# Performance work log

Hardware: AMD Instinct MI355X
Metric: run time of the kernel (lower is better)

Reference implementation:

```python
import jax, jax.numpy as jnp
import numpy as np

B, S, D, H, F = 2, 2048, 1024, 16, 4096
HD = D // H
EPS = 1e-5


def _layernorm(x, g, b):
    mu = jnp.mean(x, axis=-1, keepdims=True)
    var = jnp.var(x, axis=-1, keepdims=True)
    return (x - mu) * jax.lax.rsqrt(var + EPS) * g + b


def setup_inputs() -> dict:
    key = jax.random.key(0)
    ks = jax.random.split(key, 10)
    sd = 0.02
    return {
        "src": jax.random.normal(ks[0], (B, S, D), jnp.float32),
        "qkv_w": jax.random.normal(ks[1], (3 * D, D), jnp.float32) * sd,
        "qkv_b": jnp.zeros((3 * D,), jnp.float32),
        "out_w": jax.random.normal(ks[2], (D, D), jnp.float32) * sd,
        "out_b": jnp.zeros((D,), jnp.float32),
        "ffn_w1": jax.random.normal(ks[3], (F, D), jnp.float32) * sd,
        "ffn_b1": jnp.zeros((F,), jnp.float32),
        "ffn_w2": jax.random.normal(ks[4], (D, F), jnp.float32) * sd,
        "ffn_b2": jnp.zeros((D,), jnp.float32),
        "ln1_g": jnp.ones((D,), jnp.float32),
        "ln1_b": jnp.zeros((D,), jnp.float32),
        "ln2_g": jnp.ones((D,), jnp.float32),
        "ln2_b": jnp.zeros((D,), jnp.float32),
    }


def reference(src, qkv_w, qkv_b, out_w, out_b, ffn_w1, ffn_b1, ffn_w2, ffn_b2,
              ln1_g, ln1_b, ln2_g, ln2_b):
    # --- Multi-head self-attention (post-norm, dropout=identity in eval) ---
    qkv = src @ qkv_w.T + qkv_b                        # [B,S,3D]
    qkv = qkv.reshape(B, S, H, 3 * HD).transpose(0, 2, 1, 3)  # [B,H,S,3hd]
    q, k, v = jnp.split(qkv, 3, axis=-1)               # each [B,H,S,hd]
    scores = jnp.einsum('bhqd,bhkd->bhqk', q, k) / np.sqrt(HD).astype(np.float32)
    attn = jax.nn.softmax(scores, axis=-1)
    ctx = jnp.einsum('bhqk,bhkd->bhqd', attn, v)       # [B,H,S,hd]
    ctx = ctx.transpose(0, 2, 1, 3).reshape(B, S, D)
    mha_out = ctx @ out_w.T + out_b
    agg = _layernorm(src + mha_out, ln1_g, ln1_b)
    # --- FFN: Linear -> ReLU -> Linear ---
    h = jax.nn.relu(agg @ ffn_w1.T + ffn_b1)
    ffn_out = h @ ffn_w2.T + ffn_b2
    return _layernorm(agg + ffn_out, ln2_g, ln2_b)
```

## Files before the change

### kernel.cpp

```cpp
#include <hip/hip_runtime.h>


typedef unsigned short u16;
typedef unsigned int u32;
typedef __attribute__((ext_vector_type(8))) __bf16 bf16x8;
typedef __attribute__((ext_vector_type(4))) float f32x4;
typedef __attribute__((ext_vector_type(4))) short s16x4;
typedef __attribute__((ext_vector_type(2))) u32 u32x2;

__device__ __forceinline__ u16 f2bf(float f) {
  u32 u = __float_as_uint(f);
  u += 0x7fffu + ((u >> 16) & 1u);
  return (u16)(u >> 16);
}

__device__ __forceinline__ float bf2f(u16 h) {
  return __uint_as_float((u32)h << 16);
}

__device__ __forceinline__ u32 pk_bf_trunc(float a, float b) {
  return (__float_as_uint(a) >> 16) | (__float_as_uint(b) & 0xffff0000u);
}

__device__ __forceinline__ float exp2_fast(float x) {
  float t = __builtin_fmaf(x, 8388608.0f, 1064992506.0f);
  return __int_as_float((int)t);
}

__device__ __forceinline__ void async16(const void* g, void* l) {
  __builtin_amdgcn_global_load_lds((__attribute__((address_space(1))) void*)g,
                                   (__attribute__((address_space(3))) void*)l,
                                   16, 0, 0);
}

__device__ __forceinline__ f32x4 mfma16(bf16x8 a, bf16x8 b, f32x4 c) {
  return __builtin_amdgcn_mfma_f32_16x16x32_bf16(a, b, c, 0, 0, 0);
}

__device__ __forceinline__ f32x4 mfma_pv(s16x4 a, s16x4 b, f32x4 c) {
#if __has_builtin(__builtin_amdgcn_mfma_f32_16x16x16bf16_1k)
  return __builtin_amdgcn_mfma_f32_16x16x16bf16_1k(a, b, c, 0, 0, 0);
#else
  f32x4 d;
  asm("v_mfma_f32_16x16x16_bf16 %0, %1, %2, %3" : "=v"(d) : "v"(a), "v"(b), "v"(c));
  return d;
#endif
}

__global__ __launch_bounds__(256)
void cvt_all(const float* __restrict__ qkv_w, const float* __restrict__ out_w,
             const float* __restrict__ f1, const float* __restrict__ f2,
             const float* __restrict__ src,
             u16* __restrict__ o_qkv, u16* __restrict__ o_out,
             u16* __restrict__ o_f1, u16* __restrict__ o_f2,
             u16* __restrict__ o_src) {
  int b = blockIdx.x;
  const float* in;
  u16* out;
  int lb, ob;
  if (b < 3072) {
    int h = b / 192, c = b - h * 192;
    ob = (c < 64) ? h * 64 + c : (c < 128) ? 1024 + h * 64 + (c - 64)
                                           : 2048 + h * 64 + (c - 128);
    in = qkv_w; out = o_qkv; lb = b;
  }
  else if (b < 4096)  { in = out_w; out = o_out; lb = b - 3072;  ob = lb; }
  else if (b < 8192)  { in = f1;    out = o_f1;  lb = b - 4096;  ob = lb; }
  else if (b < 12288) { in = f2;    out = o_f2;  lb = b - 8192;  ob = lb; }
  else                { in = src;   out = o_src; lb = b - 12288; ob = lb; }
  int i = lb * 256 + threadIdx.x;
  int o = ob * 256 + threadIdx.x;
  float4 v = ((const float4*)in)[i];
  ushort4 ov;
  ov.x = f2bf(v.x); ov.y = f2bf(v.y); ov.z = f2bf(v.z); ov.w = f2bf(v.w);
  ((ushort4*)out)[o] = ov;
}

template <int MODE, int SPLIT>
__global__ __launch_bounds__(256)
void gemm_bt(const u16* __restrict__ A, const u16* __restrict__ W,
             const float* __restrict__ bias,
             u16* __restrict__ outb,
             u16* __restrict__ qo, u16* __restrict__ ko, u16* __restrict__ vto,
             int M, int N, int K) {
  __shared__ u16 As[128 * 64];
  __shared__ u16 Bs[128 * 64];
  const int lane = threadIdx.x & 63;
  const int wave = threadIdx.x >> 6;
  const int lrow = lane & 15;
  const int lq = lane >> 4;
  const int tm = blockIdx.x * 128;
  const int tn = blockIdx.y * 128;
  const int wm = (wave >> 1) * 64;
  const int wn = (wave & 1) * 64;
  const int kc = K / SPLIT;
  const int kbeg = blockIdx.z * kc;
  f32x4 acc[4][4] = {};

  for (int k0 = kbeg; k0 < kbeg + kc; k0 += 64) {
#pragma unroll
    for (int c = 0; c < 4; ++c) {
      int chunk = wave * 256 + c * 64 + lane;
      int row = chunk >> 3;
      int sc = chunk & 7;
      int cc = sc ^ (row & 7);
      u16* la = As + (size_t)(wave * 256 + c * 64) * 8;
      u16* lb = Bs + (size_t)(wave * 256 + c * 64) * 8;
      async16(A + (size_t)(tm + row) * K + (k0 + cc * 8), la);
      async16(W + (size_t)(tn + row) * K + (k0 + cc * 8), lb);
    }
    __syncthreads();
#pragma unroll
    for (int h = 0; h < 2; ++h) {
      bf16x8 a_frag[4], b_frag[4];
#pragma unroll
      for (int i = 0; i < 4; ++i) {
        int row = wm + i * 16 + lrow;
        int sc = (h * 4 + lq) ^ (row & 7);
        a_frag[i] = *(const bf16x8*)(As + row * 64 + sc * 8);
      }
#pragma unroll
      for (int j = 0; j < 4; ++j) {
        int row = wn + j * 16 + lrow;
        int sc = (h * 4 + lq) ^ (row & 7);
        b_frag[j] = *(const bf16x8*)(Bs + row * 64 + sc * 8);
      }
#pragma unroll
      for (int i = 0; i < 4; ++i)
#pragma unroll
        for (int j = 0; j < 4; ++j)
          acc[i][j] = mfma16(a_frag[i], b_frag[j], acc[i][j]);
    }
    __syncthreads();
  }

  u16* outp = outb;
  if constexpr (MODE == 0) outp += (size_t)blockIdx.z * M * N;

#pragma unroll
  for (int i = 0; i < 4; ++i) {
#pragma unroll
    for (int j = 0; j < 4; ++j) {
      int col = tn + wn + j * 16 + lrow;
      float bv = (SPLIT == 1 || blockIdx.z == 0) ? bias[col] : 0.f;
#pragma unroll
      for (int r = 0; r < 4; ++r) {
        int row = tm + wm + i * 16 + lq * 4 + r;
        float v = acc[i][j][r] + bv;
        if constexpr (MODE == 0) {
          outp[(size_t)row * N + col] = f2bf(v);
        } else {
          outp[(size_t)row * N + col] = f2bf(fmaxf(v, 0.f));
        }
      }
    }
  }
}

template <int MODE, int SPLIT>
__global__ __launch_bounds__(512, 2)
void gemm8p(const u16* __restrict__ A, const u16* __restrict__ W,
            const float* __restrict__ bias, u16* __restrict__ outb,
            u16* __restrict__ qo, u16* __restrict__ ko, u16* __restrict__ vto,
            int N, int Kfull) {
  extern __shared__ u16 lds[];
  constexpr int NTK = 16;
  constexpr int NG = NTK / 2;
  u16* As = lds;
  u16* Bs = lds + 32768;
  const int tid = threadIdx.x;
  const int lane = tid & 63;
  const int wave = tid >> 6;
  const int lrow = lane & 15;
  const int lq = lane >> 4;
  const int wm = wave >> 2;
  const int wn = wave & 3;
  const int kbeg = blockIdx.y * 1024;

  const int nwg = gridDim.x;
  const int wg = blockIdx.x;
  const int swz = (wg & 7) * (nwg >> 3) + (wg >> 3);
  const int tm = (swz & 15) * 256;
  const int tn = (swz >> 4) * 256;

  auto stage = [&](const u16* __restrict__ T, int trow0, int kt, int rbase,
                   u16* base) {
#pragma unroll
    for (int it = 0; it < 2; ++it) {
      int c = it * 512 + tid;
      int row = c >> 3, sc = c & 7, cc = sc ^ (row & 7);
      async16(T + (size_t)(trow0 + rbase + row) * Kfull + kbeg + kt * 64 + cc * 8,
              base + rbase * 64 + (it * 512 + wave * 64) * 8);
    }
  };
  auto ldA = [&](int buf, int m, int h) {
    int row = wm * 128 + m * 16 + lrow;
    int sc = (h * 4 + lq) ^ (row & 7);
    return *(const bf16x8*)(As + buf * 16384 + row * 64 + sc * 8);
  };
  auto ldB = [&](int buf, int n, int h) {
    int row = wn * 64 + n * 16 + lrow;
    int sc = (h * 4 + lq) ^ (row & 7);
    return *(const bf16x8*)(Bs + buf * 16384 + row * 64 + sc * 8);
  };

  f32x4 acc[8][4] = {};
  bf16x8 a[4][2], b[4][2];

  stage(A, tm, 0, 0, As);
  stage(A, tm, 0, 128, As);
  stage(W, tn, 0, 0, Bs);
  stage(W, tn, 0, 128, Bs);
  stage(W, tn, 1, 0, Bs + 16384);
  stage(A, tm, 1, 0, As + 16384);
  asm volatile("s_waitcnt vmcnt(4)" ::: "memory");
  __builtin_amdgcn_s_barrier();

  for (int g = 0; g < NG; ++g) {
    const int t = 2 * g;
    const int t1k = t + 1;
    const int t2k = (t + 2 < NTK) ? t + 2 : NTK - 1;
    const int t3k = (t + 3 < NTK) ? t + 3 : NTK - 1;

#pragma unroll
    for (int m = 0; m < 4; ++m) { a[m][0] = ldA(0, m, 0); a[m][1] = ldA(0, m, 1); }
#pragma unroll
    for (int n = 0; n < 2; ++n) { b[n][0] = ldB(0, n, 0); b[n][1] = ldB(0, n, 1); }
    stage(A, tm, t1k, 128, As + 16384);
    __builtin_amdgcn_s_barrier();
    asm volatile("s_waitcnt lgkmcnt(0)" ::: "memory");
    __builtin_amdgcn_s_setprio(1);
#pragma unroll
    for (int m = 0; m < 4; ++m)
#pragma unroll
      for (int n = 0; n < 2; ++n) {
        acc[m][n] = mfma16(a[m][0], b[n][0], acc[m][n]);
        acc[m][n] = mfma16(a[m][1], b[n][1], acc[m][n]);
      }
    __builtin_amdgcn_s_setprio(0);
    __builtin_amdgcn_s_barrier();

#pragma unroll
    for (int n = 0; n < 2; ++n) { b[2 + n][0] = ldB(0, 2 + n, 0); b[2 + n][1] = ldB(0, 2 + n, 1); }
    stage(W, tn, t1k, 128, Bs + 16384);
    __builtin_amdgcn_s_barrier();
    asm volatile("s_waitcnt lgkmcnt(0)" ::: "memory");
    __builtin_amdgcn_s_setprio(1);
#pragma unroll
    for (int m = 0; m < 4; ++m)
#pragma unroll
      for (int n = 0; n < 2; ++n) {
        acc[m][2 + n] = mfma16(a[m][0], b[2 + n][0], acc[m][2 + n]);
        acc[m][2 + n] = mfma16(a[m][1], b[2 + n][1], acc[m][2 + n]);
      }
    __builtin_amdgcn_s_setprio(0);
    __builtin_amdgcn_s_barrier();

#pragma unroll
    for (int m = 0; m < 4; ++m) { a[m][0] = ldA(0, 4 + m, 0); a[m][1] = ldA(0, 4 + m, 1); }
    stage(W, tn, t2k, 0, Bs);
    __builtin_amdgcn_s_barrier();
    asm volatile("s_waitcnt lgkmcnt(0)" ::: "memory");
    __builtin_amdgcn_s_setprio(1);
#pragma unroll
    for (int m = 0; m < 4; ++m)
#pragma unroll
      for (int n = 0; n < 2; ++n) {
        acc[4 + m][n] = mfma16(a[m][0], b[n][0], acc[4 + m][n]);
        acc[4 + m][n] = mfma16(a[m][1], b[n][1], acc[4 + m][n]);
      }
    __builtin_amdgcn_s_setprio(0);
    __builtin_amdgcn_s_barrier();

    stage(A, tm, t2k, 0, As);
    asm volatile("s_waitcnt vmcnt(4)" ::: "memory");
    __builtin_amdgcn_s_barrier();
    __builtin_amdgcn_s_setprio(1);
#pragma unroll
    for (int m = 0; m < 4; ++m)
#pragma unroll
      for (int n = 0; n < 2; ++n) {
        acc[4 + m][2 + n] = mfma16(a[m][0], b[2 + n][0], acc[4 + m][2 + n]);
        acc[4 + m][2 + n] = mfma16(a[m][1], b[2 + n][1], acc[4 + m][2 + n]);
      }
    __builtin_amdgcn_s_setprio(0);
    __builtin_amdgcn_s_barrier();

#pragma unroll
    for (int m = 0; m < 4; ++m) { a[m][0] = ldA(1, m, 0); a[m][1] = ldA(1, m, 1); }
#pragma unroll
    for (int n = 0; n < 2; ++n) { b[n][0] = ldB(1, n, 0); b[n][1] = ldB(1, n, 1); }
    stage(A, tm, t2k, 128, As);
    __builtin_amdgcn_s_barrier();
    asm volatile("s_waitcnt lgkmcnt(0)" ::: "memory");
    __builtin_amdgcn_s_setprio(1);
#pragma unroll
    for (int m = 0; m < 4; ++m)
#pragma unroll
      for (int n = 0; n < 2; ++n) {
        acc[m][n] = mfma16(a[m][0], b[n][0], acc[m][n]);
        acc[m][n] = mfma16(a[m][1], b[n][1], acc[m][n]);
      }
    __builtin_amdgcn_s_setprio(0);
    __builtin_amdgcn_s_barrier();

#pragma unroll
    for (int n = 0; n < 2; ++n) { b[2 + n][0] = ldB(1, 2 + n, 0); b[2 + n][1] = ldB(1, 2 + n, 1); }
    stage(W, tn, t2k, 128, Bs);
    __builtin_amdgcn_s_barrier();
    asm volatile("s_waitcnt lgkmcnt(0)" ::: "memory");
    __builtin_amdgcn_s_setprio(1);
#pragma unroll
    for (int m = 0; m < 4; ++m)
#pragma unroll
      for (int n = 0; n < 2; ++n) {
        acc[m][2 + n] = mfma16(a[m][0], b[2 + n][0], acc[m][2 + n]);
        acc[m][2 + n] = mfma16(a[m][1], b[2 + n][1], acc[m][2 + n]);
      }
    __builtin_amdgcn_s_setprio(0);
    __builtin_amdgcn_s_barrier();

#pragma unroll
    for (int m = 0; m < 4; ++m) { a[m][0] = ldA(1, 4 + m, 0); a[m][1] = ldA(1, 4 + m, 1); }
    stage(W, tn, t3k, 0, Bs + 16384);
    __builtin_amdgcn_s_barrier();
    asm volatile("s_waitcnt lgkmcnt(0)" ::: "memory");
    __builtin_amdgcn_s_setprio(1);
#pragma unroll
    for (int m = 0; m < 4; ++m)
#pragma unroll
      for (int n = 0; n < 2; ++n) {
        acc[4 + m][n] = mfma16(a[m][0], b[n][0], acc[4 + m][n]);
        acc[4 + m][n] = mfma16(a[m][1], b[n][1], acc[4 + m][n]);
      }
    __builtin_amdgcn_s_setprio(0);
    __builtin_amdgcn_s_barrier();

    stage(A, tm, t3k, 0, As + 16384);
    asm volatile("s_waitcnt vmcnt(4)" ::: "memory");
    __builtin_amdgcn_s_barrier();
    __builtin_amdgcn_s_setprio(1);
#pragma unroll
    for (int m = 0; m < 4; ++m)
#pragma unroll
      for (int n = 0; n < 2; ++n) {
        acc[4 + m][2 + n] = mfma16(a[m][0], b[2 + n][0], acc[4 + m][2 + n]);
        acc[4 + m][2 + n] = mfma16(a[m][1], b[2 + n][1], acc[4 + m][2 + n]);
      }
    __builtin_amdgcn_s_setprio(0);
    __builtin_amdgcn_s_barrier();
  }
  asm volatile("s_waitcnt vmcnt(0)" ::: "memory");
  __builtin_amdgcn_s_barrier();

  if constexpr (MODE == 0) {
    u16* outp = outb + (size_t)blockIdx.y * 4096 * N;
#pragma unroll
    for (int m = 0; m < 8; ++m)
#pragma unroll
      for (int n = 0; n < 4; ++n) {
        int col = tn + wn * 64 + n * 16 + lrow;
        float bv = (SPLIT == 1 || blockIdx.y == 0) ? bias[col] : 0.f;
#pragma unroll
        for (int r = 0; r < 4; ++r) {
          int row = tm + wm * 128 + m * 16 + lq * 4 + r;
          outp[(size_t)row * N + col] = f2bf(acc[m][n][r] + bv);
        }
      }
  } else if constexpr (MODE == 1) {
#pragma unroll
    for (int m = 0; m < 8; ++m)
#pragma unroll
      for (int n = 0; n < 4; ++n) {
        int col = tn + wn * 64 + n * 16 + lrow;
        float bv = bias[col];
#pragma unroll
        for (int r = 0; r < 4; ++r) {
          int row = tm + wm * 128 + m * 16 + lq * 4 + r;
          outb[(size_t)row * N + col] = f2bf(fmaxf(acc[m][n][r] + bv, 0.f));
        }
      }
  } else {
    const int type = tn >> 10;
    if (type < 2) {
      u16* dst = (type == 0) ? qo : ko;
      const float scale = (type == 0) ? 0.1803368801f : 1.f;
#pragma unroll
      for (int n = 0; n < 4; ++n) {
        int idx = (tn & 1023) + wn * 64 + n * 16 + lrow;
        int hh = idx >> 6, c = idx & 63;
        float bv = bias[hh * 192 + type * 64 + c];
#pragma unroll
        for (int m = 0; m < 8; ++m) {
#pragma unroll
          for (int r = 0; r < 4; ++r) {
            int row = tm + wm * 128 + m * 16 + lq * 4 + r;
            int bb = row >> 11, s = row & 2047;
            dst[(((size_t)(bb * 16 + hh) * 2048 + s) << 6) + c] =
                f2bf((acc[m][n][r] + bv) * scale);
          }
        }
      }
    } else {
      u16* T = lds + wave * 640;
      const int bb = tm >> 11;
      const int s_base = (tm & 2047) + wm * 128;
      const int idxl = lane & 15, sg = lane >> 4;
      const int idx2 = (tn & 1023) + wn * 64 + idxl;
#pragma unroll
      for (int p = 0; p < 4; ++p) {
#pragma unroll
        for (int n = 0; n < 4; ++n) {
          int idx = (tn & 1023) + wn * 64 + n * 16 + lrow;
          int hh = idx >> 6, c = idx & 63;
          float bv = bias[hh * 192 + 128 + c];
          ushort4 lo, hi;
          lo.x = f2bf(acc[2 * p][n][0] + bv);
          lo.y = f2bf(acc[2 * p][n][1] + bv);
          lo.z = f2bf(acc[2 * p][n][2] + bv);
          lo.w = f2bf(acc[2 * p][n][3] + bv);
          hi.x = f2bf(acc[2 * p + 1][n][0] + bv);
          hi.y = f2bf(acc[2 * p + 1][n][1] + bv);
          hi.z = f2bf(acc[2 * p + 1][n][2] + bv);
          hi.w = f2bf(acc[2 * p + 1][n][3] + bv);
          *(ushort4*)(T + lrow * 40 + lq * 4) = lo;
          *(ushort4*)(T + lrow * 40 + 16 + lq * 4) = hi;
          asm volatile("s_waitcnt lgkmcnt(0)" ::: "memory");
          int i2 = idx2 + n * 16;
          int hh2 = i2 >> 6, c2 = i2 & 63;
          uint4 v = *(const uint4*)(T + idxl * 40 + sg * 8);
          *(uint4*)(vto + (((size_t)(bb * 16 + hh2) * 64 + c2) << 11)
                        + s_base + p * 32 + sg * 8) = v;
          asm volatile("s_waitcnt lgkmcnt(0)" ::: "memory");
        }
      }
    }
  }
}

__global__ __launch_bounds__(512)
void attn_kernel(const u16* __restrict__ Q, const u16* __restrict__ K,
                 const u16* __restrict__ Vt,
                 u16* __restrict__ o_part, float* __restrict__ l_part) {
  extern __shared__ u16 smem[];
  u16* Ks = smem;
  u16* Vs = smem + 16384;
  const int tid = threadIdx.x;
  const int lane = tid & 63;
  const int wave = tid >> 6;
  const int wq = wave & 3;
  const int role = wave >> 2;
  const int lrow = lane & 15;
  const int q = lane >> 4;
  const int bh = blockIdx.x & 31;
  const int qb = (blockIdx.x >> 5) & 7;
  const int kvh = blockIdx.x >> 8;
  const u16* Qp = Q + ((size_t)bh * 2048 + qb * 256) * 64;
  const u16* Kp = K + (size_t)bh * 2048 * 64;
  const u16* Vp = Vt + (size_t)bh * 64 * 2048;

  bf16x8 qf[2][2];
#pragma unroll
  for (int h2 = 0; h2 < 2; ++h2)
#pragma unroll
    for (int kk = 0; kk < 2; ++kk)
      qf[h2][kk] = *(const bf16x8*)(Qp + (h2 * 128 + wave * 16 + lrow) * 64 +
                                    kk * 32 + q * 8);

  const s16x4 ones = {(short)0x3F80, (short)0x3F80, (short)0x3F80, (short)0x3F80};
  f32x4 oacc[2][4] = {};
  f32x4 lacc[2] = {};

  auto stage = [&](int kb, int buf) {
    if (role == 0) {
#pragma unroll
      for (int t = 0; t < 4; ++t) {
        int c = wq * 256 + t * 64 + lane;
        int row = c >> 3, sc = c & 7;
        int cc = sc ^ (row & 7);
        async16(Kp + (size_t)(kb * 128 + row) * 64 + cc * 8,
                Ks + buf * 8192 + (size_t)(wq * 256 + t * 64) * 8);
      }
    } else {
#pragma unroll
      for (int t = 0; t < 4; ++t) {
        int c = wq * 256 + t * 64 + lane;
        int row = c >> 4, sc = c & 15;
        int cc = sc ^ (row & 7);
        async16(Vp + (size_t)row * 2048 + kb * 128 + cc * 8,
                Vs + buf * 8192 + (size_t)(wq * 256 + t * 64) * 8);
      }
    }
  };

  const int kb0 = kvh * 8;
  stage(kb0, 0);
  asm volatile("s_waitcnt vmcnt(0)" ::: "memory");
  __builtin_amdgcn_s_barrier();

  for (int i = 0; i < 8; ++i) {
    const int buf = i & 1;
    if (i < 7) stage(kb0 + i + 1, buf ^ 1);
    const u16* Kb = Ks + buf * 8192;
    const u16* Vb = Vs + buf * 8192;

    s16x4 pa2[2][8];
#pragma unroll
    for (int h2 = 0; h2 < 2; ++h2) {
      f32x4 sacc[8] = {};
#pragma unroll
      for (int j = 0; j < 8; ++j) {
#pragma unroll
        for (int kk = 0; kk < 2; ++kk) {
          int row = j * 16 + lrow;
          int sc = (kk * 4 + q) ^ (row & 7);
          bf16x8 kf = *(const bf16x8*)(Kb + row * 64 + sc * 8);
          sacc[j] = mfma16(kf, qf[h2][kk], sacc[j]);
        }
      }
#pragma unroll
      for (int j = 0; j < 8; ++j) {
        float p0 = exp2_fast(sacc[j][0]);
        float p1 = exp2_fast(sacc[j][1]);
        float p2 = exp2_fast(sacc[j][2]);
        float p3 = exp2_fast(sacc[j][3]);
        u32x2 pw;
        pw.x = pk_bf_trunc(p0, p1);
        pw.y = pk_bf_trunc(p2, p3);
        pa2[h2][j] = __builtin_bit_cast(s16x4, pw);
      }
    }

#pragma unroll
    for (int j = 0; j < 8; ++j) {
      lacc[0] = mfma_pv(pa2[0][j], ones, lacc[0]);
      lacc[1] = mfma_pv(pa2[1][j], ones, lacc[1]);
#pragma unroll
      for (int jn = 0; jn < 4; ++jn) {
        int row = jn * 16 + lrow;
        int sc = (j * 2 + (q >> 1)) ^ (row & 7);
        s16x4 vb = *(const s16x4*)(Vb + row * 128 + sc * 8 + (q & 1) * 4);
        oacc[0][jn] = mfma_pv(pa2[0][j], vb, oacc[0][jn]);
        oacc[1][jn] = mfma_pv(pa2[1][j], vb, oacc[1][jn]);
      }
    }

    if (i < 7) {
      asm volatile("s_waitcnt vmcnt(0)" ::: "memory");
      __builtin_amdgcn_s_barrier();
    }
  }

  const int b = bh >> 4, h = bh & 15;
  u16* op = o_part + (size_t)kvh * 4096 * 1024;
  float* lp = l_part + kvh * 65536 + bh * 2048;
#pragma unroll
  for (int h2 = 0; h2 < 2; ++h2) {
#pragma unroll
    for (int r = 0; r < 4; ++r) {
      int s = qb * 256 + h2 * 128 + wave * 16 + q * 4 + r;
      if (lrow == 0) lp[s] = lacc[h2][r];
      size_t base = ((size_t)(b * 2048 + s)) * 1024 + h * 64;
#pragma unroll
      for (int jn = 0; jn < 4; ++jn)
        op[base + jn * 16 + lrow] = f2bf(oacc[h2][jn][r]);
    }
  }
}

__global__ __launch_bounds__(256)
void attn_combine(const u16* __restrict__ o_part, const float* __restrict__ l_part,
                  u16* __restrict__ ctx) {
  const int t = blockIdx.x;
  const int tid = threadIdx.x;
  __shared__ float linv[16];
  if (tid < 16) {
    int b = t >> 11, s = t & 2047;
    int bh = b * 16 + tid;
    linv[tid] = 1.f / (l_part[bh * 2048 + s] + l_part[65536 + bh * 2048 + s]);
  }
  __syncthreads();
  size_t base = (size_t)t * 1024;
  ushort4 a = ((const ushort4*)(o_part + base))[tid];
  ushort4 c = ((const ushort4*)(o_part + 4096ull * 1024 + base))[tid];
  float li = linv[tid >> 4];
  ushort4 o;
  o.x = f2bf((bf2f(a.x) + bf2f(c.x)) * li);
  o.y = f2bf((bf2f(a.y) + bf2f(c.y)) * li);
  o.z = f2bf((bf2f(a.z) + bf2f(c.z)) * li);
  o.w = f2bf((bf2f(a.w) + bf2f(c.w)) * li);
  ((ushort4*)(ctx + base))[tid] = o;
}

template <int P>
__global__ __launch_bounds__(256)
void ln_kernel(const float* __restrict__ x1, const u16* __restrict__ x2,
               const float* __restrict__ g, const float* __restrict__ bb,
               float* __restrict__ outf, u16* __restrict__ outb) {
  const int t = blockIdx.x;
  const int tid = threadIdx.x;
  const int lane = tid & 63, wave = tid >> 6;
  const size_t base = (size_t)t * 1024;
  const size_t pstride = 4096ull * 1024;
  float v[4];
  float s = 0.f, s2 = 0.f;
#pragma unroll
  for (int e = 0; e < 4; ++e) {
    int i = tid + e * 256;
    float x = x1[base + i];
#pragma unroll
    for (int p = 0; p < P; ++p) x += bf2f(x2[p * pstride + base + i]);
    v[e] = x;
    s += x;
    s2 += x * x;
  }
#pragma unroll
  for (int d = 1; d < 64; d <<= 1) {
    s += __shfl_xor(s, d);
    s2 += __shfl_xor(s2, d);
  }
  __shared__ float red[8];
  if (lane == 0) { red[wave] = s; red[4 + wave] = s2; }
  __syncthreads();
  s = red[0] + red[1] + red[2] + red[3];
  s2 = red[4] + red[5] + red[6] + red[7];
  float mean = s * (1.f / 1024.f);
  float var = s2 * (1.f / 1024.f) - mean * mean;
  float rstd = rsqrtf(var + 1e-5f);
#pragma unroll
  for (int e = 0; e < 4; ++e) {
    int i = tid + e * 256;
    float y = (v[e] - mean) * rstd * g[i] + bb[i];
    outf[base + i] = y;
    if (outb) outb[base + i] = f2bf(y);
  }
}

extern "C" void kernel_launch(void* const* d_in, const int* in_sizes, int n_in,
                              void* d_out, int out_size, void* d_ws, size_t ws_size,
                              hipStream_t stream) {
  const float* src    = (const float*)d_in[0];
  const float* qkv_w  = (const float*)d_in[1];
  const float* qkv_b  = (const float*)d_in[2];
  const float* out_w  = (const float*)d_in[3];
  const float* out_b  = (const float*)d_in[4];
  const float* ffn_w1 = (const float*)d_in[5];
  const float* ffn_b1 = (const float*)d_in[6];
  const float* ffn_w2 = (const float*)d_in[7];
  const float* ffn_b2 = (const float*)d_in[8];
  const float* ln1_g  = (const float*)d_in[9];
  const float* ln1_b  = (const float*)d_in[10];
  const float* ln2_g  = (const float*)d_in[11];
  const float* ln2_b  = (const float*)d_in[12];

  char* ws = (char*)d_ws;
  size_t off = 0;
  auto alloc = [&](size_t bytes) -> void* {
    void* p = ws + off;
    off += (bytes + 255) & ~(size_t)255;
    return p;
  };
  u16* wqkv = (u16*)alloc(3072ull * 1024 * 2);
  u16* wout = (u16*)alloc(1024ull * 1024 * 2);
  u16* wf1  = (u16*)alloc(4096ull * 1024 * 2);
  u16* wf2  = (u16*)alloc(1024ull * 4096 * 2);
  u16* srcb = (u16*)alloc(4096ull * 1024 * 2);
  u16* qb_  = (u16*)alloc(32ull * 2048 * 64 * 2);
  u16* kb_  = (u16*)alloc(32ull * 2048 * 64 * 2);
  u16* vtb  = (u16*)alloc(32ull * 64 * 2048 * 2);
  u16* opart = (u16*)alloc(2ull * 4096 * 1024 * 2);
  float* lpart = (float*)alloc(2ull * 65536 * 4);
  u16* ctxb = (u16*)alloc(4096ull * 1024 * 2);
  u16* mha  = (u16*)alloc(4ull * 4096 * 1024 * 2);
  float* aggf = (float*)alloc(4096ull * 1024 * 4);
  u16* aggb = (u16*)alloc(4096ull * 1024 * 2);
  u16* hb   = (u16*)alloc(4096ull * 4096 * 2);
  u16* ffnf = (u16*)alloc(4ull * 4096 * 1024 * 2);

  static bool attr_done = false;
  if (!attr_done) {
    auto* kq = gemm8p<2, 1>;
    auto* kf = gemm8p<1, 1>;
    auto* k2 = gemm8p<0, 4>;
    hipFuncSetAttribute(reinterpret_cast<const void*>(kq),
                        hipFuncAttributeMaxDynamicSharedMemorySize, 131072);
    hipFuncSetAttribute(reinterpret_cast<const void*>(kf),
                        hipFuncAttributeMaxDynamicSharedMemorySize, 131072);
    hipFuncSetAttribute(reinterpret_cast<const void*>(k2),
                        hipFuncAttributeMaxDynamicSharedMemorySize, 131072);
    hipFuncSetAttribute(reinterpret_cast<const void*>(attn_kernel),
                        hipFuncAttributeMaxDynamicSharedMemorySize, 65536);
    attr_done = true;
  }

  cvt_all<<<16384, 256, 0, stream>>>(qkv_w, out_w, ffn_w1, ffn_w2, src,
                                     wqkv, wout, wf1, wf2, srcb);

  gemm8p<2, 1><<<dim3(192, 1), 512, 131072, stream>>>(srcb, wqkv, qkv_b, nullptr,
                                                      qb_, kb_, vtb, 3072, 1024);
  attn_kernel<<<512, 512, 65536, stream>>>(qb_, kb_, vtb, opart, lpart);
  attn_combine<<<4096, 256, 0, stream>>>(opart, lpart, ctxb);
  gemm_bt<0, 4><<<dim3(32, 8, 4), 256, 0, stream>>>(ctxb, wout, out_b, mha,
                                                    nullptr, nullptr, nullptr, 4096, 1024, 1024);
  ln_kernel<4><<<4096, 256, 0, stream>>>(src, mha, ln1_g, ln1_b, aggf, aggb);
  gemm8p<1, 1><<<dim3(256, 1), 512, 131072, stream>>>(aggb, wf1, ffn_b1, hb,
                                                      nullptr, nullptr, nullptr, 4096, 1024);
  gemm8p<0, 4><<<dim3(64, 4), 512, 131072, stream>>>(hb, wf2, ffn_b2, ffnf,
                                                     nullptr, nullptr, nullptr, 1024, 4096);
  ln_kernel<4><<<4096, 256, 0, stream>>>(aggf, ffnf, ln2_g, ln2_b, (float*)d_out, nullptr);
}
```

Baseline: 361.4 us.

## Remap GEMM tiles per XCD and share K fragments across query halves

The GEMM workgroup-to-tile mapping changes so that each XCD owns a 4x(ntn2) block of output tiles arranged as 4x4 local groups, which is meant to improve L2 reuse of A and W within an XCD. In attention, the QK^T loop is reordered so each K fragment loaded from LDS feeds MFMAs for both query halves, halving K LDS reads. Exp/pack work is split into two batches of four. The new GEMM mapping assumes a specific grid shape (gridDim.x multiple of 32, M of 16 tiles), and the attention change may raise register pressure.

```diff
diff --git a/kernel.cpp b/kernel.cpp
--- a/kernel.cpp
+++ b/kernel.cpp
@@ -177,11 +177,11 @@
   const int wn = wave & 3;
   const int kbeg = blockIdx.y * 1024;
 
-  const int nwg = gridDim.x;
   const int wg = blockIdx.x;
-  const int swz = (wg & 7) * (nwg >> 3) + (wg >> 3);
-  const int tm = (swz & 15) * 256;
-  const int tn = (swz >> 4) * 256;
+  const int ntn2 = gridDim.x >> 5;
+  const int xcd = wg & 7, loc = wg >> 3;
+  const int tm = ((xcd & 3) * 4 + (loc & 3)) * 256;
+  const int tn = ((xcd >> 2) * ntn2 + (loc >> 2)) * 256;
 
   auto stage = [&](const u16* __restrict__ T, int trow0, int kt, int rbase,
                    u16* base) {
@@ -506,28 +506,28 @@
 
     s16x4 pa2[2][8];
 #pragma unroll
-    for (int h2 = 0; h2 < 2; ++h2) {
-      f32x4 sacc[8] = {};
-#pragma unroll
-      for (int j = 0; j < 8; ++j) {
+    for (int jb = 0; jb < 2; ++jb) {
+      f32x4 s0[4] = {}, s1[4] = {};
+#pragma unroll
+      for (int j4 = 0; j4 < 4; ++j4) {
+        int row = (jb * 4 + j4) * 16 + lrow;
 #pragma unroll
         for (int kk = 0; kk < 2; ++kk) {
-          int row = j * 16 + lrow;
           int sc = (kk * 4 + q) ^ (row & 7);
           bf16x8 kf = *(const bf16x8*)(Kb + row * 64 + sc * 8);
-          sacc[j] = mfma16(kf, qf[h2][kk], sacc[j]);
+          s0[j4] = mfma16(kf, qf[0][kk], s0[j4]);
+          s1[j4] = mfma16(kf, qf[1][kk], s1[j4]);
         }
       }
 #pragma unroll
-      for (int j = 0; j < 8; ++j) {
-        float p0 = exp2_fast(sacc[j][0]);
-        float p1 = exp2_fast(sacc[j][1]);
-        float p2 = exp2_fast(sacc[j][2]);
-        float p3 = exp2_fast(sacc[j][3]);
-        u32x2 pw;
-        pw.x = pk_bf_trunc(p0, p1);
-        pw.y = pk_bf_trunc(p2, p3);
-        pa2[h2][j] = __builtin_bit_cast(s16x4, pw);
+      for (int j4 = 0; j4 < 4; ++j4) {
+        u32x2 pw0, pw1;
+        pw0.x = pk_bf_trunc(exp2_fast(s0[j4][0]), exp2_fast(s0[j4][1]));
+        pw0.y = pk_bf_trunc(exp2_fast(s0[j4][2]), exp2_fast(s0[j4][3]));
+        pw1.x = pk_bf_trunc(exp2_fast(s1[j4][0]), exp2_fast(s1[j4][1]));
+        pw1.y = pk_bf_trunc(exp2_fast(s1[j4][2]), exp2_fast(s1[j4][3]));
+        pa2[0][jb * 4 + j4] = __builtin_bit_cast(s16x4, pw0);
+        pa2[1][jb * 4 + j4] = __builtin_bit_cast(s16x4, pw1);
       }
     }
 
```

Result: no change. 366.8 us (+1.5%).
